# Performance work log

Measured on AMD Instinct MI355X. Metric: run time of the kernel, lower is better.

The kernel has to match this reference:

```python
import jax, jax.numpy as jnp
import numpy as np

HIDDEN = 1408
HEADS = 16
HEAD_DIM = 88  # HIDDEN // HEADS
NUM_PATCHES = 576  # (336 // 14) ** 2
SEQ = NUM_PATCHES + 1  # +1 CLS token position in mllama4 rope cache
ROPE_BASE = 10000.0
SCALE = HEAD_DIM ** -0.5


def _rope_cos_sin():
    # Faithful to vLLM Llama4VisionRotaryEmbedding cos/sin cache.
    idx = np.arange(NUM_PATCHES, dtype=np.int64).reshape(NUM_PATCHES, 1)
    idx = np.concatenate([idx, idx[:1]], axis=0)
    idx[-1, -1] = -2  # CLS token id -> zero rotation
    n = int(np.sqrt(NUM_PATCHES))  # patches per side = 24
    fx = idx % n
    fy = idx // n
    rd = HEAD_DIM // 2  # rotary_dim = 44
    inv = 1.0 / ROPE_BASE ** (np.arange(0, rd, 2, dtype=np.float32) / rd)  # (22,)
    # repeat_interleave(2) then cat then [::2] == concat of the two 22-d halves
    freqs = np.concatenate(
        [(fx + 1)[..., None] * inv[None, None, :], (fy + 1)[..., None] * inv[None, None, :]],
        axis=-1,
    )  # (SEQ, 1, 44)
    freqs = np.where(idx.reshape(-1, 1, 1) < 0, 0.0, freqs).astype(np.float32)
    freqs = freqs.squeeze(1)  # (SEQ, 44)
    return jnp.asarray(np.cos(freqs)), jnp.asarray(np.sin(freqs))


_COS, _SIN = _rope_cos_sin()


def _apply_rope(x, cos, sin):
    # x: [B, S, H, D]; complex rotation over adjacent pairs (is_neox_style=False)
    B, S, H, D = x.shape
    xp = x.reshape(B, S, H, D // 2, 2)
    x0, x1 = xp[..., 0], xp[..., 1]
    c = cos[None, :, None, :]  # [1, S, 1, D//2]
    s = sin[None, :, None, :]
    out = jnp.stack([x0 * c - x1 * s, x0 * s + x1 * c], axis=-1)
    return out.reshape(B, S, H, D)


def setup_inputs() -> dict:
    key = jax.random.key(0)
    k1, k2, k3, k4, k5 = jax.random.split(key, 5)
    std = HIDDEN ** -0.5
    return {
        "hidden_states": jax.random.normal(k1, (32, SEQ, HIDDEN), dtype=jnp.float32),
        "w_qkv": jax.random.normal(k2, (HIDDEN, 3 * HIDDEN), dtype=jnp.float32) * std,
        "b_qkv": jax.random.normal(k3, (3 * HIDDEN,), dtype=jnp.float32) * 0.02,
        "w_o": jax.random.normal(k4, (HIDDEN, HIDDEN), dtype=jnp.float32) * std,
        "b_o": jax.random.normal(k5, (HIDDEN,), dtype=jnp.float32) * 0.02,
    }


def reference(hidden_states, w_qkv, b_qkv, w_o, b_o):
    B, S, _ = hidden_states.shape
    qkv = hidden_states @ w_qkv + b_qkv  # [B, S, 3*HIDDEN]
    q, k, v = jnp.split(qkv, 3, axis=-1)
    q = q.reshape(B, S, HEADS, HEAD_DIM)
    k = k.reshape(B, S, HEADS, HEAD_DIM)
    v = v.reshape(B, S, HEADS, HEAD_DIM)
    q = _apply_rope(q, _COS, _SIN)
    k = _apply_rope(k, _COS, _SIN)
    scores = jnp.einsum("bqhd,bkhd->bhqk", q, k) * SCALE
    probs = jax.nn.softmax(scores, axis=-1)
    attn = jnp.einsum("bhqk,bkhd->bqhd", probs, v).reshape(B, S, HIDDEN)
    return attn @ w_o + b_o
```

## Files before the change

### kernel.cpp

```cpp
#include <hip/hip_runtime.h>
#include <math.h>

#define HEADS    16
#define HEAD_DIM 88
#define SEQ      577
#define SEQV     640
#define HIDDEN   1408
#define NQKV     4224
#define NQKV_PAD 4352
#define NOUT_PAD 1536
#define RD       44
#define SCALE_F  0.1066003581778052f
#define MPAD_ROWS 18688
#define NT       44
#define TILE_SH  16384

typedef __attribute__((ext_vector_type(8))) short bf16x8;
typedef __attribute__((ext_vector_type(4))) float f32x4;

__device__ __forceinline__ unsigned short f2bf(float x) {
    unsigned u = __float_as_uint(x);
    unsigned r = u + 0x7fff + ((u >> 16) & 1);
    return (unsigned short)(r >> 16);
}
__device__ __forceinline__ f32x4 fzero() {
    f32x4 z; z.x = 0.f; z.y = 0.f; z.z = 0.f; z.w = 0.f; return z;
}
__device__ __forceinline__ int xcd_swz(int flat, int nwg) {
    int q = nwg >> 3, r = nwg & 7;
    int x = flat & 7, j = flat >> 3;
    return (x < r ? x * (q + 1) : r * (q + 1) + (x - r) * q) + j;
}

__global__ void rope_precompute(float* __restrict__ cosb, float* __restrict__ sinb) {
    int s = blockIdx.x;
    int j = threadIdx.x;
    if (j >= RD) return;
    float c, sn;
    if (s == SEQ - 1) {
        c = 1.f; sn = 0.f;
    } else {
        int fx = s % 24, fy = s / 24;
        int p = (j < 22) ? j : j - 22;
        float inv = powf(10000.f, -(float)p / 22.f);
        float f = (float)((j < 22 ? fx : fy) + 1) * inv;
        c = cosf(f); sn = sinf(f);
    }
    cosb[s * RD + j] = c;
    sinb[s * RD + j] = sn;
}

__global__ void conv_hs(const float* __restrict__ in, unsigned short* __restrict__ out,
                        long nreal, long ntot) {
    long i = ((long)blockIdx.x * 256 + threadIdx.x) * 4;
    if (i >= ntot) return;
    ushort4 o;
    if (i < nreal) {
        float4 v = *(const float4*)(in + i);
        o = make_ushort4(f2bf(v.x), f2bf(v.y), f2bf(v.z), f2bf(v.w));
    } else {
        o = make_ushort4(0, 0, 0, 0);
    }
    *(ushort4*)(out + i) = o;
}

__global__ void conv_wT(const float* __restrict__ in, unsigned short* __restrict__ out,
                        int R, int Creal) {
    __shared__ float t[32][33];
    int bx = blockIdx.x * 32, by = blockIdx.y * 32;
    int tx = threadIdx.x & 31, ty = threadIdx.x >> 5;
    #pragma unroll
    for (int i = 0; i < 4; ++i) {
        int col = bx + tx;
        t[ty + i * 8][tx] = (col < Creal) ? in[(size_t)(by + ty + i * 8) * Creal + col] : 0.f;
    }
    __syncthreads();
    #pragma unroll
    for (int i = 0; i < 4; ++i)
        out[(size_t)(bx + ty + i * 8) * R + by + tx] = f2bf(t[tx][ty + i * 8]);
}

__device__ __forceinline__ void stage256(const unsigned short* __restrict__ src,
                                         unsigned short* lds, int lane, int w8) {
    #pragma unroll
    for (int q = 0; q < 2; ++q) {
        int cf = lane + 64 * w8 + 512 * q;
        int r  = cf >> 2, cs = cf & 3;
        int cg = cs ^ ((r >> 1) & 3);
        __builtin_amdgcn_global_load_lds(
            (const __attribute__((address_space(1))) void*)(src + (size_t)r * HIDDEN + cg * 8),
            (__attribute__((address_space(3))) void*)(lds + (w8 + 8 * q) * 512),
            16, 0, 0);
    }
}

__device__ __forceinline__ void gemm256_main(
    const unsigned short* __restrict__ wsrc, const unsigned short* __restrict__ hsrc,
    unsigned short* smem, int tid, f32x4 (&acc)[8][4])
{
    const int lane = tid & 63, w8 = tid >> 6;
    const int quad = lane >> 4, l15 = lane & 15;
    const int ww = w8 >> 2, wh = w8 & 3;

    stage256(wsrc,      smem,                  lane, w8);
    stage256(hsrc,      smem + 8192,           lane, w8);
    stage256(wsrc + 32, smem + TILE_SH,        lane, w8);
    stage256(hsrc + 32, smem + TILE_SH + 8192, lane, w8);

    auto tile = [&](int t) {
        const unsigned short* WL = smem + (t & 3) * TILE_SH;
        const unsigned short* HL = WL + 8192;
        bf16x8 af[8], bfr[4];
        #pragma unroll
        for (int i = 0; i < 8; ++i) {
            int r = ww * 128 + i * 16 + l15;
            af[i] = *(const bf16x8*)(WL + r * 32 + ((quad ^ ((r >> 1) & 3)) << 3));
        }
        #pragma unroll
        for (int j = 0; j < 4; ++j) {
            int r = wh * 64 + j * 16 + l15;
            bfr[j] = *(const bf16x8*)(HL + r * 32 + ((quad ^ ((r >> 1) & 3)) << 3));
        }
        __builtin_amdgcn_s_setprio(1);
        #pragma unroll
        for (int i = 0; i < 8; ++i)
            #pragma unroll
            for (int j = 0; j < 4; ++j)
                acc[i][j] = __builtin_amdgcn_mfma_f32_16x16x32_bf16(
                    af[i], bfr[j], acc[i][j], 0, 0, 0);
        __builtin_amdgcn_s_setprio(0);
    };

    for (int t = 0; t < NT - 2; ++t) {
        __builtin_amdgcn_sched_barrier(0);
        stage256(wsrc + (size_t)(t + 2) * 32, smem + ((t + 2) & 3) * TILE_SH,        lane, w8);
        stage256(hsrc + (size_t)(t + 2) * 32, smem + ((t + 2) & 3) * TILE_SH + 8192, lane, w8);
        asm volatile("s_waitcnt vmcnt(8)" ::: "memory");
        __builtin_amdgcn_s_barrier();
        __builtin_amdgcn_sched_barrier(0);
        tile(t);
    }
    __builtin_amdgcn_sched_barrier(0);
    asm volatile("s_waitcnt vmcnt(4)" ::: "memory");
    __builtin_amdgcn_s_barrier();
    __builtin_amdgcn_sched_barrier(0);
    tile(NT - 2);
    __builtin_amdgcn_sched_barrier(0);
    asm volatile("s_waitcnt vmcnt(0)" ::: "memory");
    __builtin_amdgcn_s_barrier();
    __builtin_amdgcn_sched_barrier(0);
    tile(NT - 1);
}

__global__ __launch_bounds__(512, 2) void qkv_mfma(
    const unsigned short* __restrict__ hsb, const unsigned short* __restrict__ wt,
    const float* __restrict__ bias, const float* __restrict__ cosb,
    const float* __restrict__ sinb,
    unsigned short* __restrict__ qb, unsigned short* __restrict__ kb,
    unsigned short* __restrict__ vtb,
    int Mchunk, int row_off)
{
    __shared__ unsigned short smem[4 * TILE_SH];
    int tid = threadIdx.x;
    int lane = tid & 63, w8 = tid >> 6;
    int quad = lane >> 4, l15 = lane & 15;
    int ww = w8 >> 2, wh = w8 & 3;

    int nwg  = gridDim.x * gridDim.y;
    int flat = blockIdx.y * gridDim.x + blockIdx.x;
    int wg   = xcd_swz(flat, nwg);
    int n0   = (wg % gridDim.x) * 256;
    int m0   = (wg / gridDim.x) * 256;

    f32x4 acc[8][4];
    #pragma unroll
    for (int i = 0; i < 8; ++i)
        #pragma unroll
        for (int j = 0; j < 4; ++j) acc[i][j] = fzero();

    gemm256_main(wt + (size_t)n0 * HIDDEN,
                 hsb + (size_t)(row_off + m0) * HIDDEN, smem, tid, acc);

    #pragma unroll
    for (int j = 0; j < 4; ++j) {
        int m = m0 + wh * 64 + j * 16 + l15;
        if (m >= Mchunk) continue;
        int bb = m / SEQ;
        int s  = m - bb * SEQ;
        const float* cr = cosb + s * RD;
        const float* sr = sinb + s * RD;
        #pragma unroll
        for (int i = 0; i < 8; ++i) {
            int ng = n0 + ww * 128 + i * 16 + quad * 4;
            if (ng >= NQKV) continue;
            int sec = ng / HIDDEN;
            int nn  = ng - sec * HIDDEN;
            int h   = nn / HEAD_DIM;
            int d0  = nn - h * HEAD_DIM;
            int bh  = bb * HEADS + h;
            f32x4 v = acc[i][j];
            const float4 bv = *(const float4*)(bias + ng);
            v.x += bv.x; v.y += bv.y; v.z += bv.z; v.w += bv.w;
            if (sec < 2) {
                int p0 = d0 >> 1;
                float c0 = cr[p0],     s0 = sr[p0];
                float c1 = cr[p0 + 1], s1 = sr[p0 + 1];
                float x0 = v.x, x1 = v.y;
                v.x = x0 * c0 - x1 * s0; v.y = x0 * s0 + x1 * c0;
                x0 = v.z; x1 = v.w;
                v.z = x0 * c1 - x1 * s1; v.w = x0 * s1 + x1 * c1;
                if (sec == 0) { v.x *= SCALE_F; v.y *= SCALE_F; v.z *= SCALE_F; v.w *= SCALE_F; }
                unsigned short* dst = (sec == 0) ? qb : kb;
                ushort4 o = make_ushort4(f2bf(v.x), f2bf(v.y), f2bf(v.z), f2bf(v.w));
                *(ushort4*)(dst + ((size_t)bh * SEQ + s) * HEAD_DIM + d0) = o;
            } else {
                unsigned short* vb = vtb + ((size_t)bh * HEAD_DIM + d0) * SEQV + s;
                vb[0]        = f2bf(v.x);
                vb[SEQV]     = f2bf(v.y);
                vb[2 * SEQV] = f2bf(v.z);
                vb[3 * SEQV] = f2bf(v.w);
            }
        }
    }
}

__global__ __launch_bounds__(512, 2) void out_mfma(
    const unsigned short* __restrict__ ab, const unsigned short* __restrict__ wt,
    const float* __restrict__ bias, float* __restrict__ out,
    int Mchunk, int row_off)
{
    __shared__ unsigned short smem[4 * TILE_SH];
    int tid = threadIdx.x;
    int lane = tid & 63, w8 = tid >> 6;
    int quad = lane >> 4, l15 = lane & 15;
    int ww = w8 >> 2, wh = w8 & 3;

    int nwg  = gridDim.x * gridDim.y;
    int flat = blockIdx.y * gridDim.x + blockIdx.x;
    int wg   = xcd_swz(flat, nwg);
    int n0   = (wg % gridDim.x) * 256;
    int m0   = (wg / gridDim.x) * 256;

    f32x4 acc[8][4];
    #pragma unroll
    for (int i = 0; i < 8; ++i)
        #pragma unroll
        for (int j = 0; j < 4; ++j) acc[i][j] = fzero();

    gemm256_main(wt + (size_t)n0 * HIDDEN,
                 ab + (size_t)m0 * HIDDEN, smem, tid, acc);

    #pragma unroll
    for (int j = 0; j < 4; ++j) {
        int m = m0 + wh * 64 + j * 16 + l15;
        if (m >= Mchunk) continue;
        size_t orow = (size_t)(row_off + m) * HIDDEN;
        #pragma unroll
        for (int i = 0; i < 8; ++i) {
            int nn = n0 + ww * 128 + i * 16 + quad * 4;
            if (nn >= HIDDEN) continue;
            f32x4 v = acc[i][j];
            const float4 bv = *(const float4*)(bias + nn);
            v.x += bv.x; v.y += bv.y; v.z += bv.z; v.w += bv.w;
            *(f32x4*)(out + orow + nn) = v;
        }
    }
}

#define QT   128
#define KTT  64
#define KSTR 104
#define VSTR 72
#define PSTR 72
#define RESCALE_THR 8.0f

__global__ __launch_bounds__(256, 3) void attn_mfma(
    const unsigned short* __restrict__ qb, const unsigned short* __restrict__ kb,
    const unsigned short* __restrict__ vtb, unsigned short* __restrict__ awsb)
{
    __shared__ unsigned short Ks[KTT * KSTR];
    __shared__ unsigned short Vt[96 * VSTR];
    __shared__ unsigned short Ps[QT * PSTR];

    int tid = threadIdx.x;
    int lane = tid & 63, wv = tid >> 6;
    int quad = lane >> 4, l15 = lane & 15;

    int nwg  = gridDim.x * gridDim.y * gridDim.z;
    int flat = (blockIdx.z * gridDim.y + blockIdx.y) * gridDim.x + blockIdx.x;
    int w    = xcd_swz(flat, nwg);
    int qblk = w % gridDim.x;
    int rem  = w / gridDim.x;
    int h    = rem % gridDim.y;
    int bb   = rem / gridDim.y;
    int q0   = qblk * QT;
    int bh   = bb * HEADS + h;
    const unsigned short* qg = qb  + (size_t)bh * SEQ * HEAD_DIM;
    const unsigned short* kg = kb  + (size_t)bh * SEQ * HEAD_DIM;
    const unsigned short* vg = vtb + (size_t)bh * HEAD_DIM * SEQV;

    bf16x8 qf[2][3];
    #pragma unroll
    for (int mf = 0; mf < 2; ++mf)
        #pragma unroll
        for (int ks = 0; ks < 3; ++ks)
            qf[mf][ks] = *(const bf16x8*)(qg +
                (size_t)(q0 + wv * 32 + mf * 16 + l15) * HEAD_DIM + ks * 32 + quad * 8);

    f32x4 O[2][6];
    float m_i[2], l_i[2];
    #pragma unroll
    for (int mf = 0; mf < 2; ++mf) {
        #pragma unroll
        for (int nf = 0; nf < 6; ++nf) O[mf][nf] = fzero();
        m_i[mf] = -INFINITY; l_i[mf] = 0.f;
    }

    bf16x8 kr[3], vr[3];
    auto load_tile = [&](int k0) {
        #pragma unroll
        for (int it = 0; it < 3; ++it) {
            int idx = it * 256 + tid;
            int r = idx / 12, c = idx - r * 12;
            bf16x8 v = (bf16x8)(short)0;
            if (c < 11)
                v = *(const bf16x8*)(kg + (size_t)(k0 + r) * HEAD_DIM + c * 8);
            kr[it] = v;
        }
        #pragma unroll
        for (int it = 0; it < 3; ++it) {
            int idx = it * 256 + tid;
            int r = idx >> 3, c = idx & 7;
            vr[it] = *(const bf16x8*)(vg + (size_t)r * SEQV + k0 + c * 8);
        }
    };
    auto write_tile = [&]() {
        #pragma unroll
        for (int it = 0; it < 3; ++it) {
            int idx = it * 256 + tid;
            int r = idx / 12, c = idx - r * 12;
            *(bf16x8*)(Ks + r * KSTR + c * 8) = kr[it];
        }
        #pragma unroll
        for (int it = 0; it < 3; ++it) {
            int idx = it * 256 + tid;
            int r = idx >> 3, c = idx & 7;
            *(bf16x8*)(Vt + r * VSTR + c * 8) = vr[it];
        }
    };

    load_tile(0);
    write_tile();
    __syncthreads();

    for (int k0 = 0; k0 < SEQ; k0 += KTT) {
        int nxt = k0 + KTT;
        if (nxt < SEQ) load_tile(nxt);

        f32x4 sc[2][4];
        #pragma unroll
        for (int mf = 0; mf < 2; ++mf)
            #pragma unroll
            for (int nf = 0; nf < 4; ++nf) sc[mf][nf] = fzero();
        __builtin_amdgcn_s_setprio(1);
        #pragma unroll
        for (int ks = 0; ks < 3; ++ks) {
            #pragma unroll
            for (int nf = 0; nf < 4; ++nf) {
                bf16x8 a = *(const bf16x8*)(Ks + (nf * 16 + l15) * KSTR + ks * 32 + quad * 8);
                sc[0][nf] = __builtin_amdgcn_mfma_f32_16x16x32_bf16(a, qf[0][ks], sc[0][nf], 0, 0, 0);
                sc[1][nf] = __builtin_amdgcn_mfma_f32_16x16x32_bf16(a, qf[1][ks], sc[1][nf], 0, 0, 0);
            }
        }
        __builtin_amdgcn_s_setprio(0);

        #pragma unroll
        for (int mf = 0; mf < 2; ++mf) {
            float pmax = -INFINITY;
            #pragma unroll
            for (int nf = 0; nf < 4; ++nf)
                #pragma unroll
                for (int r = 0; r < 4; ++r)
                    if (k0 + nf * 16 + quad * 4 + r < SEQ)
                        pmax = fmaxf(pmax, sc[mf][nf][r]);
            pmax = fmaxf(pmax, __shfl_xor(pmax, 16));
            pmax = fmaxf(pmax, __shfl_xor(pmax, 32));
            float mold = m_i[mf];
            bool skip = __all(pmax - mold <= RESCALE_THR);
            float mnew = skip ? mold : fmaxf(mold, pmax);
            float rsum = 0.f;
            #pragma unroll
            for (int nf = 0; nf < 4; ++nf) {
                ushort4 o;
                #pragma unroll
                for (int r = 0; r < 4; ++r) {
                    bool valid = (k0 + nf * 16 + quad * 4 + r < SEQ);
                    float p = valid ? __expf(sc[mf][nf][r] - mnew) : 0.f;
                    rsum += p;
                    ((unsigned short*)&o)[r] = f2bf(p);
                }
                *(ushort4*)(Ps + (wv * 32 + mf * 16 + l15) * PSTR + nf * 16 + quad * 4) = o;
            }
            rsum += __shfl_xor(rsum, 16);
            rsum += __shfl_xor(rsum, 32);
            if (!skip) {
                float alpha = __expf(mold - mnew);
                m_i[mf] = mnew;
                l_i[mf] = l_i[mf] * alpha + rsum;
                #pragma unroll
                for (int r = 0; r < 4; ++r) {
                    float ar = __shfl(alpha, quad * 4 + r, 16);
                    #pragma unroll
                    for (int nf = 0; nf < 6; ++nf) O[mf][nf][r] *= ar;
                }
            } else {
                l_i[mf] += rsum;
            }
        }

        __builtin_amdgcn_s_setprio(1);
        #pragma unroll
        for (int ks = 0; ks < 2; ++ks) {
            bf16x8 a0 = *(const bf16x8*)(Ps + (wv * 32 + l15) * PSTR + ks * 32 + quad * 8);
            bf16x8 a1 = *(const bf16x8*)(Ps + (wv * 32 + 16 + l15) * PSTR + ks * 32 + quad * 8);
            #pragma unroll
            for (int nf = 0; nf < 6; ++nf) {
                bf16x8 b = *(const bf16x8*)(Vt + (nf * 16 + l15) * VSTR + ks * 32 + quad * 8);
                O[0][nf] = __builtin_amdgcn_mfma_f32_16x16x32_bf16(a0, b, O[0][nf], 0, 0, 0);
                O[1][nf] = __builtin_amdgcn_mfma_f32_16x16x32_bf16(a1, b, O[1][nf], 0, 0, 0);
            }
        }
        __builtin_amdgcn_s_setprio(0);

        __syncthreads();
        if (nxt < SEQ) {
            write_tile();
            __syncthreads();
        }
    }

    #pragma unroll
    for (int mf = 0; mf < 2; ++mf) {
        #pragma unroll
        for (int r = 0; r < 4; ++r) {
            int row = q0 + wv * 32 + mf * 16 + quad * 4 + r;
            if (row >= SEQ) continue;
            float lb = __shfl(l_i[mf], quad * 4 + r, 16);
            float il = 1.f / lb;
            size_t base = (size_t)(bb * SEQ + row) * HIDDEN + h * HEAD_DIM;
            #pragma unroll
            for (int nf = 0; nf < 6; ++nf) {
                int d = nf * 16 + l15;
                if (d < HEAD_DIM)
                    awsb[base + d] = f2bf(O[mf][nf][r] * il);
            }
        }
    }
}

extern "C" void kernel_launch(void* const* d_in, const int* in_sizes, int n_in,
                              void* d_out, int out_size, void* d_ws, size_t ws_size,
                              hipStream_t stream) {
    const float* hs    = (const float*)d_in[0];
    const float* w_qkv = (const float*)d_in[1];
    const float* b_qkv = (const float*)d_in[2];
    const float* w_o   = (const float*)d_in[3];
    const float* b_o   = (const float*)d_in[4];
    float* out = (float*)d_out;

    char* p = (char*)d_ws;
    auto alloc = [&](size_t bytes) {
        char* r = p; p += (bytes + 255) & ~(size_t)255; return r;
    };
    float*          cosb   = (float*)alloc((size_t)SEQ * RD * 4);
    float*          sinb   = (float*)alloc((size_t)SEQ * RD * 4);
    unsigned short* wqkv_t = (unsigned short*)alloc((size_t)NQKV_PAD * HIDDEN * 2);
    unsigned short* wo_t   = (unsigned short*)alloc((size_t)NOUT_PAD * HIDDEN * 2);
    unsigned short* hs_bf  = (unsigned short*)alloc((size_t)MPAD_ROWS * HIDDEN * 2);
    size_t fixed = (size_t)(p - (char*)d_ws);

    size_t per_batch = 2ull * HEADS * SEQ * HEAD_DIM * 2
                     + (size_t)HEADS * HEAD_DIM * SEQV * 2
                     + (size_t)SEQ * HIDDEN * 2;
    size_t pads = 2ull * 64 * HEAD_DIM * 2 + 16ull * SEQV * 2 + 256ull * HIDDEN * 2 + 16 * 256;
    size_t rem = (ws_size > fixed + pads) ? ws_size - fixed - pads : 0;
    int CB = (int)(rem / per_batch);
    if (CB < 1) CB = 1;
    if (CB > 32) CB = 32;

    unsigned short* qbuf  = (unsigned short*)alloc(((size_t)CB * HEADS * SEQ + 64) * HEAD_DIM * 2);
    unsigned short* kbuf  = (unsigned short*)alloc(((size_t)CB * HEADS * SEQ + 64) * HEAD_DIM * 2);
    unsigned short* vtbuf = (unsigned short*)alloc(((size_t)CB * HEADS * HEAD_DIM + 16) * SEQV * 2);
    unsigned short* awsb  = (unsigned short*)alloc(((size_t)CB * SEQ + 256) * HIDDEN * 2);

    rope_precompute<<<dim3(SEQ), dim3(64), 0, stream>>>(cosb, sinb);

    long nreal = (long)32 * SEQ * HIDDEN;
    long ntot  = (long)MPAD_ROWS * HIDDEN;
    conv_hs<<<dim3((unsigned)((ntot / 4 + 255) / 256)), 256, 0, stream>>>(hs, hs_bf, nreal, ntot);
    conv_wT<<<dim3(NQKV_PAD / 32, HIDDEN / 32), 256, 0, stream>>>(w_qkv, wqkv_t, HIDDEN, NQKV);
    conv_wT<<<dim3(NOUT_PAD / 32, HIDDEN / 32), 256, 0, stream>>>(w_o, wo_t, HIDDEN, HIDDEN);

    for (int b_off = 0; b_off < 32; b_off += CB) {
        int nb = (32 - b_off < CB) ? (32 - b_off) : CB;
        int M = nb * SEQ;

        dim3 g1(NQKV_PAD / 256, (M + 255) / 256);
        qkv_mfma<<<g1, 512, 0, stream>>>(hs_bf, wqkv_t, b_qkv, cosb, sinb,
                                         qbuf, kbuf, vtbuf, M, b_off * SEQ);
        dim3 g2((SEQ + QT - 1) / QT, HEADS, nb);
        attn_mfma<<<g2, 256, 0, stream>>>(qbuf, kbuf, vtbuf, awsb);
        dim3 g3(NOUT_PAD / 256, (M + 255) / 256);
        out_mfma<<<g3, 512, 0, stream>>>(awsb, wo_t, b_o, out, M, b_off * SEQ);
    }
}
```

Before: 766.4 us.

## Restructure 256x256 GEMM mainloop into 8-phase quadrant schedule with K=64 tiles

Replaces the four-buffer K=32 pipeline in the shared QKV and output GEMMs with a two-buffer K=64 scheme. Each K-tile is split into four quadrant sub-phases that interleave half-tile global-to-LDS staging with MFMA work, and the LDS swizzle is changed to an 8-chunk XOR. Warp-to-output mapping changes so that each warp owns a 64x32 sub-block per quadrant, and the epilogue index math is updated to match. The goal is finer overlap of loads with MFMAs and fewer barrier iterations, at the cost of more barriers per K-tile and a complex hand-tuned vmcnt schedule that is fragile to get right.

```diff
diff --git a/kernel.cpp b/kernel.cpp
--- a/kernel.cpp
+++ b/kernel.cpp
@@ -12,8 +12,8 @@
 #define RD       44
 #define SCALE_F  0.1066003581778052f
 #define MPAD_ROWS 18688
-#define NT       44
-#define TILE_SH  16384
+#define NKT      22
+#define BUF_SH   32768
 
 typedef __attribute__((ext_vector_type(8))) short bf16x8;
 typedef __attribute__((ext_vector_type(4))) float f32x4;
@@ -80,21 +80,72 @@
         out[(size_t)(bx + ty + i * 8) * R + by + tx] = f2bf(t[tx][ty + i * 8]);
 }
 
-__device__ __forceinline__ void stage256(const unsigned short* __restrict__ src,
-                                         unsigned short* lds, int lane, int w8) {
+__device__ __forceinline__ void stage_half(const unsigned short* __restrict__ src,
+                                           int kt, unsigned short* lds, int tid) {
     #pragma unroll
     for (int q = 0; q < 2; ++q) {
-        int cf = lane + 64 * w8 + 512 * q;
-        int r  = cf >> 2, cs = cf & 3;
-        int cg = cs ^ ((r >> 1) & 3);
+        int cf = tid + 512 * q;
+        int r  = cf >> 3, c = cf & 7;
+        int cg = c ^ (r & 7);
         __builtin_amdgcn_global_load_lds(
-            (const __attribute__((address_space(1))) void*)(src + (size_t)r * HIDDEN + cg * 8),
-            (__attribute__((address_space(3))) void*)(lds + (w8 + 8 * q) * 512),
+            (const __attribute__((address_space(1))) void*)(src + (size_t)r * HIDDEN + kt * 64 + cg * 8),
+            (__attribute__((address_space(3))) void*)(lds + cf * 8),
             16, 0, 0);
     }
 }
 
-__device__ __forceinline__ void gemm256_main(
+template<int N> __device__ __forceinline__ void vwait() {
+    if constexpr (N >= 0)
+        asm volatile("s_waitcnt vmcnt(%0)" :: "i"(N) : "memory");
+}
+
+template<int CBUF, int IH, int JH, bool STG, int SSIDE, int SHALF, int SBUF, int WAITN>
+__device__ __forceinline__ void phase8(
+    const unsigned short* __restrict__ wsrc, const unsigned short* __restrict__ hsrc,
+    unsigned short* smem, int skt, int tid,
+    int ww, int wh, int quad, int l15, f32x4 (&acc)[8][4])
+{
+    bf16x8 afr[4][2], bfr[2][2];
+    #pragma unroll
+    for (int i2 = 0; i2 < 4; ++i2)
+        #pragma unroll
+        for (int kk = 0; kk < 2; ++kk) {
+            int r = ww * 64 + i2 * 16 + l15;
+            afr[i2][kk] = *(const bf16x8*)(smem + CBUF * BUF_SH + IH * 8192
+                          + r * 64 + (((kk * 4 + quad) ^ (r & 7)) << 3));
+        }
+    #pragma unroll
+    for (int j2 = 0; j2 < 2; ++j2)
+        #pragma unroll
+        for (int kk = 0; kk < 2; ++kk) {
+            int r = wh * 32 + j2 * 16 + l15;
+            bfr[j2][kk] = *(const bf16x8*)(smem + CBUF * BUF_SH + 16384 + JH * 8192
+                          + r * 64 + (((kk * 4 + quad) ^ (r & 7)) << 3));
+        }
+    if constexpr (STG) {
+        const unsigned short* s = (SSIDE ? hsrc : wsrc) + (size_t)SHALF * 128 * HIDDEN;
+        stage_half(s, skt, smem + SBUF * BUF_SH + (SSIDE ? 16384 : 0) + SHALF * 8192, tid);
+    }
+    __builtin_amdgcn_sched_barrier(0);
+    __builtin_amdgcn_s_barrier();
+    __builtin_amdgcn_sched_barrier(0);
+    __builtin_amdgcn_s_setprio(1);
+    #pragma unroll
+    for (int i2 = 0; i2 < 4; ++i2)
+        #pragma unroll
+        for (int j2 = 0; j2 < 2; ++j2)
+            #pragma unroll
+            for (int kk = 0; kk < 2; ++kk)
+                acc[IH * 4 + i2][JH * 2 + j2] = __builtin_amdgcn_mfma_f32_16x16x32_bf16(
+                    afr[i2][kk], bfr[j2][kk], acc[IH * 4 + i2][JH * 2 + j2], 0, 0, 0);
+    __builtin_amdgcn_s_setprio(0);
+    __builtin_amdgcn_sched_barrier(0);
+    vwait<WAITN>();
+    __builtin_amdgcn_s_barrier();
+    __builtin_amdgcn_sched_barrier(0);
+}
+
+__device__ __forceinline__ void gemm256_8ph(
     const unsigned short* __restrict__ wsrc, const unsigned short* __restrict__ hsrc,
     unsigned short* smem, int tid, f32x4 (&acc)[8][4])
 {
@@ -102,54 +153,35 @@
     const int quad = lane >> 4, l15 = lane & 15;
     const int ww = w8 >> 2, wh = w8 & 3;
 
-    stage256(wsrc,      smem,                  lane, w8);
-    stage256(hsrc,      smem + 8192,           lane, w8);
-    stage256(wsrc + 32, smem + TILE_SH,        lane, w8);
-    stage256(hsrc + 32, smem + TILE_SH + 8192, lane, w8);
-
-    auto tile = [&](int t) {
-        const unsigned short* WL = smem + (t & 3) * TILE_SH;
-        const unsigned short* HL = WL + 8192;
-        bf16x8 af[8], bfr[4];
-        #pragma unroll
-        for (int i = 0; i < 8; ++i) {
-            int r = ww * 128 + i * 16 + l15;
-            af[i] = *(const bf16x8*)(WL + r * 32 + ((quad ^ ((r >> 1) & 3)) << 3));
-        }
-        #pragma unroll
-        for (int j = 0; j < 4; ++j) {
-            int r = wh * 64 + j * 16 + l15;
-            bfr[j] = *(const bf16x8*)(HL + r * 32 + ((quad ^ ((r >> 1) & 3)) << 3));
-        }
-        __builtin_amdgcn_s_setprio(1);
-        #pragma unroll
-        for (int i = 0; i < 8; ++i)
-            #pragma unroll
-            for (int j = 0; j < 4; ++j)
-                acc[i][j] = __builtin_amdgcn_mfma_f32_16x16x32_bf16(
-                    af[i], bfr[j], acc[i][j], 0, 0, 0);
-        __builtin_amdgcn_s_setprio(0);
-    };
-
-    for (int t = 0; t < NT - 2; ++t) {
-        __builtin_amdgcn_sched_barrier(0);
-        stage256(wsrc + (size_t)(t + 2) * 32, smem + ((t + 2) & 3) * TILE_SH,        lane, w8);
-        stage256(hsrc + (size_t)(t + 2) * 32, smem + ((t + 2) & 3) * TILE_SH + 8192, lane, w8);
-        asm volatile("s_waitcnt vmcnt(8)" ::: "memory");
-        __builtin_amdgcn_s_barrier();
-        __builtin_amdgcn_sched_barrier(0);
-        tile(t);
-    }
-    __builtin_amdgcn_sched_barrier(0);
+    stage_half(wsrc,                0, smem,                  tid);
+    stage_half(hsrc,                0, smem + 16384,          tid);
+    stage_half(wsrc + 128 * HIDDEN, 0, smem + 8192,           tid);
+    stage_half(hsrc + 128 * HIDDEN, 0, smem + 24576,          tid);
+    stage_half(wsrc,                1, smem + BUF_SH,         tid);
+    stage_half(hsrc,                1, smem + BUF_SH + 16384, tid);
     asm volatile("s_waitcnt vmcnt(4)" ::: "memory");
     __builtin_amdgcn_s_barrier();
     __builtin_amdgcn_sched_barrier(0);
-    tile(NT - 2);
-    __builtin_amdgcn_sched_barrier(0);
-    asm volatile("s_waitcnt vmcnt(0)" ::: "memory");
-    __builtin_amdgcn_s_barrier();
-    __builtin_amdgcn_sched_barrier(0);
-    tile(NT - 1);
+
+    for (int it = 0; it < 10; ++it) {
+        int k1 = 2 * it + 1, k2 = 2 * it + 2, k3 = 2 * it + 3;
+        phase8<0,0,0, true,0,1,1,  6>(wsrc, hsrc, smem, k1, tid, ww, wh, quad, l15, acc);
+        phase8<0,0,1, true,1,1,1, -1>(wsrc, hsrc, smem, k1, tid, ww, wh, quad, l15, acc);
+        phase8<0,1,0, true,0,0,0, -1>(wsrc, hsrc, smem, k2, tid, ww, wh, quad, l15, acc);
+        phase8<0,1,1, true,1,0,0,  8>(wsrc, hsrc, smem, k2, tid, ww, wh, quad, l15, acc);
+        phase8<1,0,0, true,0,1,0,  6>(wsrc, hsrc, smem, k2, tid, ww, wh, quad, l15, acc);
+        phase8<1,0,1, true,1,1,0, -1>(wsrc, hsrc, smem, k2, tid, ww, wh, quad, l15, acc);
+        phase8<1,1,0, true,0,0,1, -1>(wsrc, hsrc, smem, k3, tid, ww, wh, quad, l15, acc);
+        phase8<1,1,1, true,1,0,1,  8>(wsrc, hsrc, smem, k3, tid, ww, wh, quad, l15, acc);
+    }
+    phase8<0,0,0, true,0,1,1,  6>(wsrc, hsrc, smem, 21, tid, ww, wh, quad, l15, acc);
+    phase8<0,0,1, true,1,1,1, -1>(wsrc, hsrc, smem, 21, tid, ww, wh, quad, l15, acc);
+    phase8<0,1,0, false,0,0,0, -1>(wsrc, hsrc, smem, 0, tid, ww, wh, quad, l15, acc);
+    phase8<0,1,1, false,0,0,0,  4>(wsrc, hsrc, smem, 0, tid, ww, wh, quad, l15, acc);
+    phase8<1,0,0, false,0,0,0,  0>(wsrc, hsrc, smem, 0, tid, ww, wh, quad, l15, acc);
+    phase8<1,0,1, false,0,0,0, -1>(wsrc, hsrc, smem, 0, tid, ww, wh, quad, l15, acc);
+    phase8<1,1,0, false,0,0,0, -1>(wsrc, hsrc, smem, 0, tid, ww, wh, quad, l15, acc);
+    phase8<1,1,1, false,0,0,0, -1>(wsrc, hsrc, smem, 0, tid, ww, wh, quad, l15, acc);
 }
 
 __global__ __launch_bounds__(512, 2) void qkv_mfma(
@@ -160,7 +192,7 @@
     unsigned short* __restrict__ vtb,
     int Mchunk, int row_off)
 {
-    __shared__ unsigned short smem[4 * TILE_SH];
+    __shared__ unsigned short smem[2 * BUF_SH];
     int tid = threadIdx.x;
     int lane = tid & 63, w8 = tid >> 6;
     int quad = lane >> 4, l15 = lane & 15;
@@ -178,12 +210,12 @@
         #pragma unroll
         for (int j = 0; j < 4; ++j) acc[i][j] = fzero();
 
-    gemm256_main(wt + (size_t)n0 * HIDDEN,
-                 hsb + (size_t)(row_off + m0) * HIDDEN, smem, tid, acc);
+    gemm256_8ph(wt + (size_t)n0 * HIDDEN,
+                hsb + (size_t)(row_off + m0) * HIDDEN, smem, tid, acc);
 
     #pragma unroll
     for (int j = 0; j < 4; ++j) {
-        int m = m0 + wh * 64 + j * 16 + l15;
+        int m = m0 + (j >> 1) * 128 + wh * 32 + (j & 1) * 16 + l15;
         if (m >= Mchunk) continue;
         int bb = m / SEQ;
         int s  = m - bb * SEQ;
@@ -191,7 +223,7 @@
         const float* sr = sinb + s * RD;
         #pragma unroll
         for (int i = 0; i < 8; ++i) {
-            int ng = n0 + ww * 128 + i * 16 + quad * 4;
+            int ng = n0 + (i >> 2) * 128 + ww * 64 + (i & 3) * 16 + quad * 4;
             if (ng >= NQKV) continue;
             int sec = ng / HIDDEN;
             int nn  = ng - sec * HIDDEN;
@@ -229,7 +261,7 @@
     const float* __restrict__ bias, float* __restrict__ out,
     int Mchunk, int row_off)
 {
-    __shared__ unsigned short smem[4 * TILE_SH];
+    __shared__ unsigned short smem[2 * BUF_SH];
     int tid = threadIdx.x;
     int lane = tid & 63, w8 = tid >> 6;
     int quad = lane >> 4, l15 = lane & 15;
@@ -247,17 +279,17 @@
         #pragma unroll
         for (int j = 0; j < 4; ++j) acc[i][j] = fzero();
 
-    gemm256_main(wt + (size_t)n0 * HIDDEN,
-                 ab + (size_t)m0 * HIDDEN, smem, tid, acc);
+    gemm256_8ph(wt + (size_t)n0 * HIDDEN,
+                ab + (size_t)m0 * HIDDEN, smem, tid, acc);
 
     #pragma unroll
     for (int j = 0; j < 4; ++j) {
-        int m = m0 + wh * 64 + j * 16 + l15;
+        int m = m0 + (j >> 1) * 128 + wh * 32 + (j & 1) * 16 + l15;
         if (m >= Mchunk) continue;
         size_t orow = (size_t)(row_off + m) * HIDDEN;
         #pragma unroll
         for (int i = 0; i < 8; ++i) {
-            int nn = n0 + ww * 128 + i * 16 + quad * 4;
+            int nn = n0 + (i >> 2) * 128 + ww * 64 + (i & 3) * 16 + quad * 4;
             if (nn >= HIDDEN) continue;
             f32x4 v = acc[i][j];
             const float4 bv = *(const float4*)(bias + nn);
```

New measurement: 776.8 us. About the same (+1.4%).
